# Kernel optimization log

Measured on AMD Instinct MI355X. Metric: run time of the kernel, lower is better.

## Reference

```python
import jax, jax.numpy as jnp
import numpy as np

B, C = 4096, 128
EPS_BN = 1e-5  # torch BatchNorm1d default eps
EPS_ATT = 1e-9


def setup_inputs() -> dict:
    key = jax.random.key(0)
    ks = jax.random.split(key, 6)
    x1 = jax.random.normal(ks[0], (B, C, 1), jnp.float32)
    x2 = jax.random.normal(ks[1], (B, C, 1), jnp.float32)
    x1_2 = jax.random.normal(ks[2], (B, C, 1), jnp.float32)
    # trans_conv: Conv1d(C, C, kernel_size=1) -> weight (C_out, C_in)
    conv_w = jax.random.normal(ks[3], (C, C), jnp.float32) / np.sqrt(C).astype(np.float32)
    conv_b = jnp.zeros((C,), jnp.float32)
    # BatchNorm1d(C) affine params
    bn_gamma = jnp.ones((C,), jnp.float32)
    bn_beta = jnp.zeros((C,), jnp.float32)
    # fc_relation: Linear(2C+1, 1)
    fc_w = jax.random.normal(ks[4], (1, 2 * C + 1), jnp.float32) / np.sqrt(2 * C + 1).astype(np.float32)
    fc_b = jnp.zeros((1,), jnp.float32)
    return {"x1": x1, "x2": x2, "x1_2": x1_2, "conv_w": conv_w, "conv_b": conv_b,
            "bn_gamma": bn_gamma, "bn_beta": bn_beta, "fc_w": fc_w, "fc_b": fc_b}


def reference(x1, x2, x1_2, conv_w, conv_b, bn_gamma, bn_beta, fc_w, fc_b):
    # energy = bmm(x1, x2^T): (B,C,1) x (B,1,C) -> (B,C,C) outer product
    energy = jnp.einsum('bcl,bdl->bcd', x1, x2)
    energy = jax.nn.softmax(energy, axis=-1)
    # normalize columns (sum over dim=1)
    attention = energy / (EPS_ATT + energy.sum(axis=1, keepdims=True))
    # x_r = bmm(attention, x1_2): (B,C,C) x (B,C,1) -> (B,C,1)
    x_r = jnp.einsum('bcd,bdl->bcl', attention, x1_2)
    # 1x1 conv = per-position channel mixing
    t = jnp.einsum('oc,bcl->bol', conv_w, x_r) + conv_b[None, :, None]
    y = x1 - t
    # BatchNorm1d in training mode: per-channel stats over (batch, length)
    mean = y.mean(axis=(0, 2), keepdims=True)          # (1,C,1)
    var = y.var(axis=(0, 2), keepdims=True)            # biased variance
    y = (y - mean) * jax.lax.rsqrt(var + EPS_BN)
    y = y * bn_gamma[None, :, None] + bn_beta[None, :, None]
    x_r_out = jax.nn.relu(y)                            # (B,C,1)
    # gated fusion: cat([energy, energy^T, x1], dim=2) -> (B, C, 2C+1)
    feat = jnp.concatenate([energy, jnp.swapaxes(energy, 1, 2), x1], axis=2)
    gate = jax.nn.sigmoid(jnp.einsum('bcf,of->bco', feat, fc_w) + fc_b)  # (B,C,1)
    return gate * x1 + x_r_out
```

## Files before the change

### kernel.cpp

```cpp
#include <hip/hip_runtime.h>

#define B_ 4096
#define C_ 128
#define EPS_ATT 1e-9f
#define EPS_BN 1e-5f
#define LOG2E 1.44269504088896f

using short8 = __attribute__((ext_vector_type(8))) short;
using f32x4 = __attribute__((ext_vector_type(4))) float;
using u32x2 = __attribute__((ext_vector_type(2))) unsigned int;

__device__ __forceinline__ unsigned short bf16b(float x) {
    __bf16 h = (__bf16)x;
    return __builtin_bit_cast(unsigned short, h);
}

__global__ __launch_bounds__(256, 4) void k_batch(
    const float* __restrict__ x1, const float* __restrict__ x2,
    const float* __restrict__ x12,
    const float* __restrict__ fcw, const float* __restrict__ fcb,
    float* __restrict__ XR, float* __restrict__ GX1) {
    const int b = blockIdx.x;
    const int tid = threadIdx.x;
    const int lane = tid & 63;
    const int w = tid >> 6;
    const int g = lane >> 4;
    const int ls = lane & 15;

    __shared__ char s_buf[C_ * C_ * 2] __attribute__((aligned(16)));
    __shared__ float s_x1[C_] __attribute__((aligned(16)));
    __shared__ float s_x2[C_] __attribute__((aligned(16)));
    __shared__ float s_fcC[C_] __attribute__((aligned(16)));
    __shared__ float s_invZ[C_] __attribute__((aligned(16)));
    __shared__ float s_cs4[4][C_] __attribute__((aligned(16)));
    __shared__ float s_s24[4][C_] __attribute__((aligned(16)));
    __shared__ unsigned short s_f1bf[C_] __attribute__((aligned(16)));

    float* s_S1 = (float*)s_buf;
    float* s_xrr = (float*)(s_buf + 512);
    unsigned short* s_w3bf = (unsigned short*)(s_buf + 1024);

    float v12 = 0.f;
    if (tid < C_) {
        s_x1[tid] = x1[b * C_ + tid];
        s_x2[tid] = x2[b * C_ + tid];
        s_f1bf[tid] = bf16b(fcw[tid]);
        s_fcC[tid] = fcw[C_ + tid];
        v12 = x12[b * C_ + tid];
    }
    __syncthreads();

    short8 ef0[4], ef1[4];
    float zp0 = 0.f, zp1 = 0.f;
    {
        const float r0 = s_x1[32 * w + ls] * LOG2E;
        const float r1 = s_x1[32 * w + 16 + ls] * LOG2E;
        char* erow0 = s_buf + (32 * w + ls) * 256;
        char* erow1 = s_buf + (32 * w + 16 + ls) * 256;
        const int sw = (ls & 7) << 4;
#pragma unroll
        for (int q = 0; q < 4; ++q) {
            f32x4 xa = *(const f32x4*)&s_x2[32 * q + 8 * g];
            f32x4 xb = *(const f32x4*)&s_x2[32 * q + 8 * g + 4];
            union {
                short8 v;
                unsigned short u[8];
            } p0, p1;
#pragma unroll
            for (int j = 0; j < 4; ++j) {
                float a0 = __builtin_amdgcn_exp2f(r0 * xa[j]);
                float b0 = __builtin_amdgcn_exp2f(r0 * xb[j]);
                float a1 = __builtin_amdgcn_exp2f(r1 * xa[j]);
                float b1 = __builtin_amdgcn_exp2f(r1 * xb[j]);
                zp0 += a0 + b0;
                zp1 += a1 + b1;
                p0.u[j] = bf16b(a0);
                p0.u[j + 4] = bf16b(b0);
                p1.u[j] = bf16b(a1);
                p1.u[j + 4] = bf16b(b1);
            }
            ef0[q] = p0.v;
            ef1[q] = p1.v;
            const int off = (64 * q + 16 * g) ^ sw;
            *(short8*)(erow0 + off) = p0.v;
            *(short8*)(erow1 + off) = p1.v;
        }
    }
    zp0 += __shfl_xor(zp0, 16);
    zp0 += __shfl_xor(zp0, 32);
    zp1 += __shfl_xor(zp1, 16);
    zp1 += __shfl_xor(zp1, 32);
    if (lane < 16) {
        s_invZ[32 * w + ls] = 1.f / zp0;
        s_invZ[32 * w + 16 + ls] = 1.f / zp1;
    }
    __syncthreads();

    {
        const int grp = tid & 31;
        const int sl = tid >> 5;
        const char* eb = s_buf + sl * 16 * 256;
        const int octb = grp >> 1;
        const int hoff = (grp & 1) * 8;
        float cs[4] = {0.f, 0.f, 0.f, 0.f};
        float s2[4] = {0.f, 0.f, 0.f, 0.f};
#pragma unroll
        for (int k = 0; k < 4; ++k) {
            f32x4 iz4 = *(const f32x4*)&s_invZ[sl * 16 + 4 * k];
            f32x4 fc4 = *(const f32x4*)&s_fcC[sl * 16 + 4 * k];
#pragma unroll
            for (int rr = 0; rr < 4; ++rr) {
                const int r = 4 * k + rr;
                const float iz = iz4[rr];
                const float izf = iz * fc4[rr];
                u32x2 ev = *(const u32x2*)(eb + r * 256 +
                                           ((octb ^ (r & 7)) << 4) + hoff);
#pragma unroll
                for (int d = 0; d < 2; ++d) {
                    float elo = __builtin_bit_cast(float, ev[d] << 16);
                    float ehi =
                        __builtin_bit_cast(float, ev[d] & 0xffff0000u);
                    cs[2 * d] = fmaf(elo, iz, cs[2 * d]);
                    s2[2 * d] = fmaf(elo, izf, s2[2 * d]);
                    cs[2 * d + 1] = fmaf(ehi, iz, cs[2 * d + 1]);
                    s2[2 * d + 1] = fmaf(ehi, izf, s2[2 * d + 1]);
                }
            }
        }
#pragma unroll
        for (int k = 0; k < 4; ++k) {
            cs[k] += __shfl_xor(cs[k], 32);
            s2[k] += __shfl_xor(s2[k], 32);
        }
        if ((sl & 1) == 0) {
            f32x4 c4 = {cs[0], cs[1], cs[2], cs[3]};
            f32x4 t4 = {s2[0], s2[1], s2[2], s2[3]};
            *(f32x4*)&s_cs4[w][grp * 4] = c4;
            *(f32x4*)&s_s24[w][grp * 4] = t4;
        }
    }
    __syncthreads();

    if (tid < C_) {
        float cs = s_cs4[0][tid] + s_cs4[1][tid] + s_cs4[2][tid] + s_cs4[3][tid];
        float w3 = v12 / (EPS_ATT + cs);
        s_w3bf[tid] = bf16b(w3);
    }
    __syncthreads();

    {
        const short8 z8 = {0, 0, 0, 0, 0, 0, 0, 0};
        short8 bq[4];
#pragma unroll
        for (int q = 0; q < 4; ++q) {
            if (ls == 0)
                bq[q] = *(const short8*)&s_f1bf[q * 32 + g * 8];
            else if (ls == 1)
                bq[q] = *(const short8*)&s_w3bf[q * 32 + g * 8];
            else
                bq[q] = z8;
        }
        f32x4 acc0 = {0.f, 0.f, 0.f, 0.f};
        f32x4 acc1 = {0.f, 0.f, 0.f, 0.f};
#pragma unroll
        for (int q = 0; q < 4; ++q) {
            acc0 = __builtin_amdgcn_mfma_f32_16x16x32_bf16(ef0[q], bq[q], acc0, 0, 0, 0);
            acc1 = __builtin_amdgcn_mfma_f32_16x16x32_bf16(ef1[q], bq[q], acc1, 0, 0, 0);
        }
        if (ls < 2) {
            float* dst = ls ? s_xrr : s_S1;
            *(f32x4*)&dst[(2 * w + 0) * 16 + g * 4] = acc0;
            *(f32x4*)&dst[(2 * w + 1) * 16 + g * 4] = acc1;
        }
    }
    __syncthreads();

    if (tid < C_) {
        float invz = s_invZ[tid];
        float S1 = s_S1[tid] * invz;
        float xr = s_xrr[tid] * invz;
        float S2 = s_s24[0][tid] + s_s24[1][tid] + s_s24[2][tid] + s_s24[3][tid];
        XR[b * C_ + tid] = xr;
        float gg = S1 + S2 + s_x1[tid] * fcw[2 * C_] + fcb[0];
        float gate = 1.f / (1.f + __builtin_amdgcn_exp2f(-LOG2E * gg));
        GX1[b * C_ + tid] = gate * s_x1[tid];
    }
}

__global__ __launch_bounds__(512, 2) void k_conv(
    const float* __restrict__ W, const float* __restrict__ XR,
    const float* __restrict__ x1, const float* __restrict__ convb,
    float* __restrict__ Y, float* __restrict__ pst) {
    const int blk = blockIdx.x;
    const int tid = threadIdx.x;
    const int bb = blk * 16;

    __shared__ float s_W[C_ * C_] __attribute__((aligned(16)));
    __shared__ float s_xr[16 * C_] __attribute__((aligned(16)));
    __shared__ float s_tp[2 * 16 * C_] __attribute__((aligned(16)));

#pragma unroll
    for (int k = 0; k < 32; ++k) {
        int j = k * 512 + tid;
        int o = j >> 7, i = j & 127;
        s_W[i * C_ + (o ^ (i & 28))] = W[j];
    }
#pragma unroll
    for (int k = 0; k < 4; ++k) {
        int j = k * 512 + tid;
        s_xr[j] = XR[bb * C_ + j];
    }
    __syncthreads();

    const int q = tid & 31;
    const int sub = (tid >> 5) & 7;
    const int ih = tid >> 8;
    const int bl0 = 2 * sub, bl1 = bl0 + 1;
    {
        f32x4 a0 = {0.f, 0.f, 0.f, 0.f};
        f32x4 a1 = {0.f, 0.f, 0.f, 0.f};
#pragma unroll
        for (int iq = 0; iq < 16; ++iq) {
            const int i0 = ih * 64 + 4 * iq;
            f32x4 xv0 = *(const f32x4*)&s_xr[bl0 * C_ + i0];
            f32x4 xv1 = *(const f32x4*)&s_xr[bl1 * C_ + i0];
#pragma unroll
            for (int u = 0; u < 4; ++u) {
                const int i = i0 + u;
                f32x4 wv = *(const f32x4*)&s_W[i * C_ + ((4 * q) ^ (i & 28))];
                a0[0] = fmaf(wv[0], xv0[u], a0[0]);
                a0[1] = fmaf(wv[1], xv0[u], a0[1]);
                a0[2] = fmaf(wv[2], xv0[u], a0[2]);
                a0[3] = fmaf(wv[3], xv0[u], a0[3]);
                a1[0] = fmaf(wv[0], xv1[u], a1[0]);
                a1[1] = fmaf(wv[1], xv1[u], a1[1]);
                a1[2] = fmaf(wv[2], xv1[u], a1[2]);
                a1[3] = fmaf(wv[3], xv1[u], a1[3]);
            }
        }
        *(f32x4*)&s_tp[(ih * 16 + bl0) * C_ + 4 * q] = a0;
        *(f32x4*)&s_tp[(ih * 16 + bl1) * C_ + 4 * q] = a1;
    }
    __syncthreads();

    float* s_sa = s_W;
    float* s_sb = s_W + 16 * C_;
    {
        const int bl = tid >> 5;
        const int gb = bb + bl;
        f32x4 t4 = *(const f32x4*)&s_tp[bl * C_ + 4 * q];
        f32x4 t4b = *(const f32x4*)&s_tp[(16 + bl) * C_ + 4 * q];
        f32x4 cb = *(const f32x4*)&convb[4 * q];
        f32x4 xv = *(const f32x4*)&x1[gb * C_ + 4 * q];
        f32x4 y;
#pragma unroll
        for (int u = 0; u < 4; ++u) y[u] = xv[u] - (t4[u] + t4b[u] + cb[u]);
        *(f32x4*)&Y[gb * C_ + 4 * q] = y;
        *(f32x4*)&s_sa[bl * C_ + 4 * q] = y;
        f32x4 y2;
#pragma unroll
        for (int u = 0; u < 4; ++u) y2[u] = y[u] * y[u];
        *(f32x4*)&s_sb[bl * C_ + 4 * q] = y2;
    }
    __syncthreads();

    if (tid < 64) {
        const int qq = tid & 31;
        const float* src = (tid < 32) ? s_sa : s_sb;
        f32x4 acc = {0.f, 0.f, 0.f, 0.f};
#pragma unroll
        for (int bl = 0; bl < 16; ++bl)
            acc += *(const f32x4*)&src[bl * C_ + 4 * qq];
        float* dst = pst + (tid < 32 ? 0 : C_ * 256);
#pragma unroll
        for (int j = 0; j < 4; ++j) dst[(4 * qq + j) * 256 + blk] = acc[j];
    }
}

__global__ __launch_bounds__(1024) void k_final(const float* __restrict__ Y,
                                                const float* __restrict__ pst,
                                                const float* __restrict__ gamma,
                                                const float* __restrict__ beta,
                                                float* __restrict__ out) {
    const int t = threadIdx.x;
    const int i4 = blockIdx.x * 1024 + t;
    float4 y = ((const float4*)Y)[i4];
    float4 o = ((const float4*)out)[i4];

    __shared__ float s_red[2][4][C_];
    __shared__ float sA[C_];
    __shared__ float sB[C_];
    {
        const int ch = t & 127;
        const int seg = (t >> 7) & 3;
        const int arr = t >> 9;
        const float* src = pst + arr * (C_ * 256) + ch * 256 + seg * 64;
        f32x4 a = {0.f, 0.f, 0.f, 0.f};
#pragma unroll
        for (int k = 0; k < 16; ++k) a += *(const f32x4*)&src[4 * k];
        s_red[arr][seg][ch] = (a[0] + a[1]) + (a[2] + a[3]);
    }
    __syncthreads();
    if (t < C_) {
        float s = s_red[0][0][t] + s_red[0][1][t] + s_red[0][2][t] + s_red[0][3][t];
        float qv = s_red[1][0][t] + s_red[1][1][t] + s_red[1][2][t] + s_red[1][3][t];
        float mean = s * (1.f / (float)B_);
        float var = qv * (1.f / (float)B_) - mean * mean;
        float A = gamma[t] * rsqrtf(var + EPS_BN);
        sA[t] = A;
        sB[t] = beta[t] - mean * A;
    }
    __syncthreads();
    const int ch = (4 * t) & (C_ - 1);
    o.x += fmaxf(y.x * sA[ch + 0] + sB[ch + 0], 0.f);
    o.y += fmaxf(y.y * sA[ch + 1] + sB[ch + 1], 0.f);
    o.z += fmaxf(y.z * sA[ch + 2] + sB[ch + 2], 0.f);
    o.w += fmaxf(y.w * sA[ch + 3] + sB[ch + 3], 0.f);
    ((float4*)out)[i4] = o;
}

extern "C" void kernel_launch(void* const* d_in, const int* in_sizes, int n_in,
                              void* d_out, int out_size, void* d_ws,
                              size_t ws_size, hipStream_t stream) {
    const float* x1 = (const float*)d_in[0];
    const float* x2 = (const float*)d_in[1];
    const float* x12 = (const float*)d_in[2];
    const float* convw = (const float*)d_in[3];
    const float* convb = (const float*)d_in[4];
    const float* gamma = (const float*)d_in[5];
    const float* beta = (const float*)d_in[6];
    const float* fcw = (const float*)d_in[7];
    const float* fcb = (const float*)d_in[8];
    float* out = (float*)d_out;

    float* XR = (float*)d_ws;
    float* Y = XR + (size_t)B_ * C_;
    float* pst = Y + (size_t)B_ * C_;

    k_batch<<<B_, 256, 0, stream>>>(x1, x2, x12, fcw, fcb, XR, out);
    k_conv<<<256, 512, 0, stream>>>(convw, XR, x1, convb, Y, pst);
    k_final<<<(B_ * C_ / 4) / 1024, 1024, 0, stream>>>(Y, pst, gamma, beta, out);
}
```

Baseline: 40.48 us.

## Transpose energy tile in registers via identity-matrix MFMA instead of LDS

Stops staging the full 128x128 bf16 energy tile in shared memory for the column-sum pass. Each wave instead multiplies its register-resident energy fragments by a bf16 identity matrix with MFMA to bring them into a column-major layout, then reduces column sums with FMAs and cross-lane shuffles. This removes 32 KB of LDS traffic and LDS footprint, which may allow more resident blocks. The cost is extra MFMA and shuffle work per block.

```diff
diff --git a/kernel.cpp b/kernel.cpp
--- a/kernel.cpp
+++ b/kernel.cpp
@@ -8,7 +8,6 @@
 
 using short8 = __attribute__((ext_vector_type(8))) short;
 using f32x4 = __attribute__((ext_vector_type(4))) float;
-using u32x2 = __attribute__((ext_vector_type(2))) unsigned int;
 
 __device__ __forceinline__ unsigned short bf16b(float x) {
     __bf16 h = (__bf16)x;
@@ -27,18 +26,17 @@
     const int g = lane >> 4;
     const int ls = lane & 15;
 
-    __shared__ char s_buf[C_ * C_ * 2] __attribute__((aligned(16)));
     __shared__ float s_x1[C_] __attribute__((aligned(16)));
     __shared__ float s_x2[C_] __attribute__((aligned(16)));
     __shared__ float s_fcC[C_] __attribute__((aligned(16)));
     __shared__ float s_invZ[C_] __attribute__((aligned(16)));
+    __shared__ float s_izf[C_] __attribute__((aligned(16)));
     __shared__ float s_cs4[4][C_] __attribute__((aligned(16)));
     __shared__ float s_s24[4][C_] __attribute__((aligned(16)));
+    __shared__ float s_S1[C_] __attribute__((aligned(16)));
+    __shared__ float s_xrr[C_] __attribute__((aligned(16)));
+    __shared__ unsigned short s_w3bf[C_] __attribute__((aligned(16)));
     __shared__ unsigned short s_f1bf[C_] __attribute__((aligned(16)));
-
-    float* s_S1 = (float*)s_buf;
-    float* s_xrr = (float*)(s_buf + 512);
-    unsigned short* s_w3bf = (unsigned short*)(s_buf + 1024);
 
     float v12 = 0.f;
     if (tid < C_) {
@@ -55,9 +53,6 @@
     {
         const float r0 = s_x1[32 * w + ls] * LOG2E;
         const float r1 = s_x1[32 * w + 16 + ls] * LOG2E;
-        char* erow0 = s_buf + (32 * w + ls) * 256;
-        char* erow1 = s_buf + (32 * w + 16 + ls) * 256;
-        const int sw = (ls & 7) << 4;
 #pragma unroll
         for (int q = 0; q < 4; ++q) {
             f32x4 xa = *(const f32x4*)&s_x2[32 * q + 8 * g];
@@ -81,9 +76,6 @@
             }
             ef0[q] = p0.v;
             ef1[q] = p1.v;
-            const int off = (64 * q + 16 * g) ^ sw;
-            *(short8*)(erow0 + off) = p0.v;
-            *(short8*)(erow1 + off) = p1.v;
         }
     }
     zp0 += __shfl_xor(zp0, 16);
@@ -91,52 +83,56 @@
     zp1 += __shfl_xor(zp1, 16);
     zp1 += __shfl_xor(zp1, 32);
     if (lane < 16) {
-        s_invZ[32 * w + ls] = 1.f / zp0;
-        s_invZ[32 * w + 16 + ls] = 1.f / zp1;
-    }
-    __syncthreads();
-
-    {
-        const int grp = tid & 31;
-        const int sl = tid >> 5;
-        const char* eb = s_buf + sl * 16 * 256;
-        const int octb = grp >> 1;
-        const int hoff = (grp & 1) * 8;
-        float cs[4] = {0.f, 0.f, 0.f, 0.f};
-        float s2[4] = {0.f, 0.f, 0.f, 0.f};
-#pragma unroll
-        for (int k = 0; k < 4; ++k) {
-            f32x4 iz4 = *(const f32x4*)&s_invZ[sl * 16 + 4 * k];
-            f32x4 fc4 = *(const f32x4*)&s_fcC[sl * 16 + 4 * k];
-#pragma unroll
-            for (int rr = 0; rr < 4; ++rr) {
-                const int r = 4 * k + rr;
-                const float iz = iz4[rr];
-                const float izf = iz * fc4[rr];
-                u32x2 ev = *(const u32x2*)(eb + r * 256 +
-                                           ((octb ^ (r & 7)) << 4) + hoff);
-#pragma unroll
-                for (int d = 0; d < 2; ++d) {
-                    float elo = __builtin_bit_cast(float, ev[d] << 16);
-                    float ehi =
-                        __builtin_bit_cast(float, ev[d] & 0xffff0000u);
-                    cs[2 * d] = fmaf(elo, iz, cs[2 * d]);
-                    s2[2 * d] = fmaf(elo, izf, s2[2 * d]);
-                    cs[2 * d + 1] = fmaf(ehi, iz, cs[2 * d + 1]);
-                    s2[2 * d + 1] = fmaf(ehi, izf, s2[2 * d + 1]);
+        const int r0 = 32 * w + ls, r1 = r0 + 16;
+        float iz0 = 1.f / zp0, iz1 = 1.f / zp1;
+        s_invZ[r0] = iz0;
+        s_invZ[r1] = iz1;
+        s_izf[r0] = iz0 * s_fcC[r0];
+        s_izf[r1] = iz1 * s_fcC[r1];
+    }
+    __syncthreads();
+
+    {
+        union BI {
+            unsigned short u[8];
+            short8 v;
+        };
+        BI b0i, b1i;
+#pragma unroll
+        for (int j = 0; j < 8; ++j) {
+            const int k = 8 * g + j;
+            b0i.u[j] = (k == ls) ? (unsigned short)0x3F80 : (unsigned short)0;
+            b1i.u[j] = (k == 16 + ls) ? (unsigned short)0x3F80 : (unsigned short)0;
+        }
+        const f32x4 iz0 = *(const f32x4*)&s_invZ[32 * w + 4 * g];
+        const f32x4 iz1 = *(const f32x4*)&s_invZ[32 * w + 16 + 4 * g];
+        const f32x4 zf0 = *(const f32x4*)&s_izf[32 * w + 4 * g];
+        const f32x4 zf1 = *(const f32x4*)&s_izf[32 * w + 16 + 4 * g];
+        const f32x4 zero = {0.f, 0.f, 0.f, 0.f};
+#pragma unroll
+        for (int q = 0; q < 4; ++q) {
+#pragma unroll
+            for (int h = 0; h < 2; ++h) {
+                const short8 bb = h ? b1i.v : b0i.v;
+                f32x4 d0 = __builtin_amdgcn_mfma_f32_16x16x32_bf16(ef0[q], bb, zero, 0, 0, 0);
+                f32x4 d1 = __builtin_amdgcn_mfma_f32_16x16x32_bf16(ef1[q], bb, zero, 0, 0, 0);
+                float cs = 0.f, s2 = 0.f;
+#pragma unroll
+                for (int r = 0; r < 4; ++r) {
+                    cs = fmaf(iz0[r], d0[r], cs);
+                    cs = fmaf(iz1[r], d1[r], cs);
+                    s2 = fmaf(zf0[r], d0[r], s2);
+                    s2 = fmaf(zf1[r], d1[r], s2);
+                }
+                cs += __shfl_xor(cs, 16);
+                cs += __shfl_xor(cs, 32);
+                s2 += __shfl_xor(s2, 16);
+                s2 += __shfl_xor(s2, 32);
+                if (g == 0) {
+                    s_cs4[w][32 * q + 16 * h + ls] = cs;
+                    s_s24[w][32 * q + 16 * h + ls] = s2;
                 }
             }
-        }
-#pragma unroll
-        for (int k = 0; k < 4; ++k) {
-            cs[k] += __shfl_xor(cs[k], 32);
-            s2[k] += __shfl_xor(s2[k], 32);
-        }
-        if ((sl & 1) == 0) {
-            f32x4 c4 = {cs[0], cs[1], cs[2], cs[3]};
-            f32x4 t4 = {s2[0], s2[1], s2[2], s2[3]};
-            *(f32x4*)&s_cs4[w][grp * 4] = c4;
-            *(f32x4*)&s_s24[w][grp * 4] = t4;
         }
     }
     __syncthreads();
```

After: 42.76 us. 1.06x slower.

## Fuse conv and batchnorm-final into one kernel with grid barrier and bf16 MFMA

Applied to the files above, without the earlier changes.

Merges the conv and final batchnorm kernels into a single kernel that keeps Y in shared memory and uses an atomic-counter grid barrier across its 256 blocks to finish the batch statistics. The kernel launch is removed, along with the Y round trip through global memory. The 1x1 conv is now done with bf16 MFMA instead of fp32 FMAs, and per-block partial sums are reduced with warp shuffles. This lowers precision of the conv and relies on all 256 blocks being co-resident for the spin barrier.

```diff
diff --git a/kernel.cpp b/kernel.cpp
--- a/kernel.cpp
+++ b/kernel.cpp
@@ -8,6 +8,7 @@
 
 using short8 = __attribute__((ext_vector_type(8))) short;
 using f32x4 = __attribute__((ext_vector_type(4))) float;
+using us4 = __attribute__((ext_vector_type(4))) unsigned short;
 using u32x2 = __attribute__((ext_vector_type(2))) unsigned int;
 
 __device__ __forceinline__ unsigned short bf16b(float x) {
@@ -19,9 +20,11 @@
     const float* __restrict__ x1, const float* __restrict__ x2,
     const float* __restrict__ x12,
     const float* __restrict__ fcw, const float* __restrict__ fcb,
-    float* __restrict__ XR, float* __restrict__ GX1) {
+    float* __restrict__ XR, float* __restrict__ GX1,
+    unsigned int* __restrict__ cnt) {
     const int b = blockIdx.x;
     const int tid = threadIdx.x;
+    if (b == 0 && tid == 0) *cnt = 0u;
     const int lane = tid & 63;
     const int w = tid >> 6;
     const int g = lane >> 4;
@@ -187,136 +190,129 @@
     }
 }
 
-__global__ __launch_bounds__(512, 2) void k_conv(
+__global__ __launch_bounds__(512) void k_cf(
     const float* __restrict__ W, const float* __restrict__ XR,
     const float* __restrict__ x1, const float* __restrict__ convb,
-    float* __restrict__ Y, float* __restrict__ pst) {
+    const float* __restrict__ gamma, const float* __restrict__ beta,
+    float* __restrict__ pst, unsigned int* __restrict__ cnt,
+    float* __restrict__ out) {
     const int blk = blockIdx.x;
     const int tid = threadIdx.x;
     const int bb = blk * 16;
-
-    __shared__ float s_W[C_ * C_] __attribute__((aligned(16)));
-    __shared__ float s_xr[16 * C_] __attribute__((aligned(16)));
-    __shared__ float s_tp[2 * 16 * C_] __attribute__((aligned(16)));
-
-#pragma unroll
-    for (int k = 0; k < 32; ++k) {
-        int j = k * 512 + tid;
-        int o = j >> 7, i = j & 127;
-        s_W[i * C_ + (o ^ (i & 28))] = W[j];
-    }
-#pragma unroll
-    for (int k = 0; k < 4; ++k) {
-        int j = k * 512 + tid;
-        s_xr[j] = XR[bb * C_ + j];
-    }
-    __syncthreads();
-
-    const int q = tid & 31;
-    const int sub = (tid >> 5) & 7;
-    const int ih = tid >> 8;
-    const int bl0 = 2 * sub, bl1 = bl0 + 1;
-    {
-        f32x4 a0 = {0.f, 0.f, 0.f, 0.f};
-        f32x4 a1 = {0.f, 0.f, 0.f, 0.f};
-#pragma unroll
-        for (int iq = 0; iq < 16; ++iq) {
-            const int i0 = ih * 64 + 4 * iq;
-            f32x4 xv0 = *(const f32x4*)&s_xr[bl0 * C_ + i0];
-            f32x4 xv1 = *(const f32x4*)&s_xr[bl1 * C_ + i0];
-#pragma unroll
-            for (int u = 0; u < 4; ++u) {
-                const int i = i0 + u;
-                f32x4 wv = *(const f32x4*)&s_W[i * C_ + ((4 * q) ^ (i & 28))];
-                a0[0] = fmaf(wv[0], xv0[u], a0[0]);
-                a0[1] = fmaf(wv[1], xv0[u], a0[1]);
-                a0[2] = fmaf(wv[2], xv0[u], a0[2]);
-                a0[3] = fmaf(wv[3], xv0[u], a0[3]);
-                a1[0] = fmaf(wv[0], xv1[u], a1[0]);
-                a1[1] = fmaf(wv[1], xv1[u], a1[1]);
-                a1[2] = fmaf(wv[2], xv1[u], a1[2]);
-                a1[3] = fmaf(wv[3], xv1[u], a1[3]);
+    const int lane = tid & 63;
+    const int wid = tid >> 6;
+    const int g = lane >> 4;
+    const int ls = lane & 15;
+
+    __shared__ unsigned short s_Wb[C_ * C_] __attribute__((aligned(16)));
+    __shared__ unsigned short s_xrb[16 * 136] __attribute__((aligned(16)));
+    __shared__ float s_Y[16 * C_] __attribute__((aligned(16)));
+    __shared__ float s_A[C_] __attribute__((aligned(16)));
+    __shared__ float s_B[C_] __attribute__((aligned(16)));
+
+    {
+        const int r = tid >> 2;
+        const int c0 = (tid & 3) * 4;
+        const float* src = W + r * C_ + c0 * 8;
+#pragma unroll
+        for (int c = 0; c < 4; ++c) {
+            f32x4 a = *(const f32x4*)(src + c * 8);
+            f32x4 b2 = *(const f32x4*)(src + c * 8 + 4);
+            union {
+                short8 v;
+                unsigned short u[8];
+            } p;
+#pragma unroll
+            for (int j = 0; j < 4; ++j) {
+                p.u[j] = bf16b(a[j]);
+                p.u[j + 4] = bf16b(b2[j]);
             }
-        }
-        *(f32x4*)&s_tp[(ih * 16 + bl0) * C_ + 4 * q] = a0;
-        *(f32x4*)&s_tp[(ih * 16 + bl1) * C_ + 4 * q] = a1;
-    }
-    __syncthreads();
-
-    float* s_sa = s_W;
-    float* s_sb = s_W + 16 * C_;
-    {
-        const int bl = tid >> 5;
-        const int gb = bb + bl;
-        f32x4 t4 = *(const f32x4*)&s_tp[bl * C_ + 4 * q];
-        f32x4 t4b = *(const f32x4*)&s_tp[(16 + bl) * C_ + 4 * q];
-        f32x4 cb = *(const f32x4*)&convb[4 * q];
-        f32x4 xv = *(const f32x4*)&x1[gb * C_ + 4 * q];
-        f32x4 y;
-#pragma unroll
-        for (int u = 0; u < 4; ++u) y[u] = xv[u] - (t4[u] + t4b[u] + cb[u]);
-        *(f32x4*)&Y[gb * C_ + 4 * q] = y;
-        *(f32x4*)&s_sa[bl * C_ + 4 * q] = y;
-        f32x4 y2;
-#pragma unroll
-        for (int u = 0; u < 4; ++u) y2[u] = y[u] * y[u];
-        *(f32x4*)&s_sb[bl * C_ + 4 * q] = y2;
-    }
-    __syncthreads();
-
-    if (tid < 64) {
-        const int qq = tid & 31;
-        const float* src = (tid < 32) ? s_sa : s_sb;
+            *(short8*)&s_Wb[r * C_ + (((c0 + c) ^ (r & 7)) << 3)] = p.v;
+        }
+    }
+    {
+        const int r = tid >> 5;
+        const int c = (tid & 31) * 4;
+        f32x4 a = *(const f32x4*)&XR[(bb + r) * C_ + c];
+        us4 p;
+#pragma unroll
+        for (int j = 0; j < 4; ++j) p[j] = bf16b(a[j]);
+        *(us4*)&s_xrb[r * 136 + c] = p;
+    }
+    __syncthreads();
+
+    {
+        const int n = 16 * wid + ls;
+        short8 aq[4], bq[4];
+#pragma unroll
+        for (int q = 0; q < 4; ++q) {
+            aq[q] = *(const short8*)&s_xrb[ls * 136 + 32 * q + 8 * g];
+            bq[q] = *(const short8*)&s_Wb[n * C_ + (((4 * q + g) ^ (n & 7)) << 3)];
+        }
         f32x4 acc = {0.f, 0.f, 0.f, 0.f};
 #pragma unroll
-        for (int bl = 0; bl < 16; ++bl)
-            acc += *(const f32x4*)&src[bl * C_ + 4 * qq];
-        float* dst = pst + (tid < 32 ? 0 : C_ * 256);
-#pragma unroll
-        for (int j = 0; j < 4; ++j) dst[(4 * qq + j) * 256 + blk] = acc[j];
-    }
-}
-
-__global__ __launch_bounds__(1024) void k_final(const float* __restrict__ Y,
-                                                const float* __restrict__ pst,
-                                                const float* __restrict__ gamma,
-                                                const float* __restrict__ beta,
-                                                float* __restrict__ out) {
-    const int t = threadIdx.x;
-    const int i4 = blockIdx.x * 1024 + t;
-    float4 y = ((const float4*)Y)[i4];
-    float4 o = ((const float4*)out)[i4];
-
-    __shared__ float s_red[2][4][C_];
-    __shared__ float sA[C_];
-    __shared__ float sB[C_];
-    {
-        const int ch = t & 127;
-        const int seg = (t >> 7) & 3;
-        const int arr = t >> 9;
-        const float* src = pst + arr * (C_ * 256) + ch * 256 + seg * 64;
+        for (int q = 0; q < 4; ++q)
+            acc = __builtin_amdgcn_mfma_f32_16x16x32_bf16(aq[q], bq[q], acc, 0, 0, 0);
+
+        const float cbv = convb[n];
+        float ps = 0.f, pq = 0.f;
+#pragma unroll
+        for (int r = 0; r < 4; ++r) {
+            const int m = 4 * g + r;
+            float y = x1[(bb + m) * C_ + n] - (acc[r] + cbv);
+            s_Y[m * C_ + n] = y;
+            ps += y;
+            pq += y * y;
+        }
+        ps += __shfl_xor(ps, 16);
+        ps += __shfl_xor(ps, 32);
+        pq += __shfl_xor(pq, 16);
+        pq += __shfl_xor(pq, 32);
+        if (lane < 16) {
+            pst[n * 256 + blk] = ps;
+            pst[32768 + n * 256 + blk] = pq;
+        }
+    }
+
+    __threadfence();
+    __syncthreads();
+    if (tid == 0) {
+        atomicAdd(cnt, 1u);
+        while (atomicAdd(cnt, 0u) < 256u) __builtin_amdgcn_s_sleep(2);
+    }
+    __syncthreads();
+    __threadfence();
+
+    if (tid < 256) {
+        const int arr = tid >> 7, ch = tid & 127;
+        const float* src = pst + arr * 32768 + ch * 256;
         f32x4 a = {0.f, 0.f, 0.f, 0.f};
 #pragma unroll
-        for (int k = 0; k < 16; ++k) a += *(const f32x4*)&src[4 * k];
-        s_red[arr][seg][ch] = (a[0] + a[1]) + (a[2] + a[3]);
-    }
-    __syncthreads();
-    if (t < C_) {
-        float s = s_red[0][0][t] + s_red[0][1][t] + s_red[0][2][t] + s_red[0][3][t];
-        float qv = s_red[1][0][t] + s_red[1][1][t] + s_red[1][2][t] + s_red[1][3][t];
-        float mean = s * (1.f / (float)B_);
-        float var = qv * (1.f / (float)B_) - mean * mean;
-        float A = gamma[t] * rsqrtf(var + EPS_BN);
-        sA[t] = A;
-        sB[t] = beta[t] - mean * A;
-    }
-    __syncthreads();
-    const int ch = (4 * t) & (C_ - 1);
-    o.x += fmaxf(y.x * sA[ch + 0] + sB[ch + 0], 0.f);
-    o.y += fmaxf(y.y * sA[ch + 1] + sB[ch + 1], 0.f);
-    o.z += fmaxf(y.z * sA[ch + 2] + sB[ch + 2], 0.f);
-    o.w += fmaxf(y.w * sA[ch + 3] + sB[ch + 3], 0.f);
-    ((float4*)out)[i4] = o;
+        for (int k = 0; k < 64; ++k) a += *(const f32x4*)&src[4 * k];
+        float tot = (a[0] + a[1]) + (a[2] + a[3]);
+        (arr ? s_B : s_A)[ch] = tot;
+    }
+    __syncthreads();
+    if (tid < C_) {
+        float mean = s_A[tid] * (1.f / (float)B_);
+        float var = s_B[tid] * (1.f / (float)B_) - mean * mean;
+        float Aa = gamma[tid] * rsqrtf(var + EPS_BN);
+        s_A[tid] = Aa;
+        s_B[tid] = beta[tid] - mean * Aa;
+    }
+    __syncthreads();
+
+    {
+        const int r = tid >> 5;
+        const int c = (tid & 31) * 4;
+        f32x4 y = *(const f32x4*)&s_Y[r * C_ + c];
+        float* op = out + (bb + r) * C_ + c;
+        f32x4 o = *(const f32x4*)op;
+#pragma unroll
+        for (int u = 0; u < 4; ++u)
+            o[u] += fmaxf(y[u] * s_A[c + u] + s_B[c + u], 0.f);
+        *(f32x4*)op = o;
+    }
 }
 
 extern "C" void kernel_launch(void* const* d_in, const int* in_sizes, int n_in,
@@ -334,10 +330,9 @@
     float* out = (float*)d_out;
 
     float* XR = (float*)d_ws;
-    float* Y = XR + (size_t)B_ * C_;
-    float* pst = Y + (size_t)B_ * C_;
-
-    k_batch<<<B_, 256, 0, stream>>>(x1, x2, x12, fcw, fcb, XR, out);
-    k_conv<<<256, 512, 0, stream>>>(convw, XR, x1, convb, Y, pst);
-    k_final<<<(B_ * C_ / 4) / 1024, 1024, 0, stream>>>(Y, pst, gamma, beta, out);
+    float* pst = XR + (size_t)B_ * C_;
+    unsigned int* cnt = (unsigned int*)(pst + 2 * C_ * 256);
+
+    k_batch<<<B_, 256, 0, stream>>>(x1, x2, x12, fcw, fcb, XR, out, cnt);
+    k_cf<<<256, 512, 0, stream>>>(convw, XR, x1, convb, gamma, beta, pst, cnt, out);
 }
```

After: 134.1 us. 3.31x slower.
